# Performance work log

Hardware: AMD Instinct MI355X
Metric: run time of the kernel (lower is better)

## Reference

```python
import jax, jax.numpy as jnp
import numpy as np

N_NODES = 100000
N_EDGES = 3200000
N_FEAT = 128
N_GRAPHS = 1024
N_CLASSES = 10
K = 30  # global_sort_pool k


def setup_inputs() -> dict:
    key = jax.random.key(0)
    ks = jax.random.split(key, 20)
    p = lambda k, shape: jax.random.normal(k, shape, jnp.float32) * 0.1
    return {
        "x": jax.random.normal(ks[0], (N_NODES, N_FEAT), jnp.float32),
        "w1": p(ks[1], (N_FEAT, 32)), "b1": p(ks[2], (32,)),
        "w2": p(ks[3], (32, 32)),     "b2": p(ks[4], (32,)),
        "w3": p(ks[5], (32, 32)),     "b3": p(ks[6], (32,)),
        "w4": p(ks[7], (32, 1)),      "b4": p(ks[8], (1,)),
        "conv5_w": p(ks[9], (16, 1, 97)),  "conv5_b": p(ks[10], (16,)),
        "conv6_w": p(ks[11], (32, 16, 5)), "conv6_b": p(ks[12], (32,)),
        "fc1_w": p(ks[13], (352, 128)),    "fc1_b": p(ks[14], (128,)),
        "fc2_w": p(ks[15], (128, N_CLASSES)), "fc2_b": p(ks[16], (N_CLASSES,)),
        "edge_src": jax.random.randint(ks[17], (N_EDGES,), 0, N_NODES),
        "edge_dst": jax.random.randint(ks[18], (N_EDGES,), 0, N_NODES),
        "batch": jnp.sort(jax.random.randint(ks[19], (N_NODES,), 0, N_GRAPHS)),
        "num_graphs": N_GRAPHS,
    }


def _gcn_forward(x, w1, b1, w2, b2, w3, b3, w4, b4,
                 conv5_w, conv5_b, conv6_w, conv6_b,
                 fc1_w, fc1_b, fc2_w, fc2_b,
                 edge_src, edge_dst, batch, num_graphs):
    n = x.shape[0]
    # remove_self_loops: mask self-loop edges to weight 0 (shapes stay static)
    ew = (edge_src != edge_dst).astype(x.dtype)
    # gcn_norm with added self-loops (weight 1): deg includes self-loop
    deg = jax.ops.segment_sum(ew, edge_dst, num_segments=n) + 1.0
    dis = jax.lax.rsqrt(deg)                       # deg^{-1/2}
    enorm = dis[edge_src] * dis[edge_dst] * ew     # [E]
    snorm = (dis * dis)[:, None]                   # self-loop norm [n,1]

    def gcn_conv(h, W, b):
        h = h @ W                                   # [n, out]
        agg = jax.ops.segment_sum(h[edge_src] * enorm[:, None], edge_dst,
                                  num_segments=n) + h * snorm
        return agg + b

    x1 = jnp.tanh(gcn_conv(x,  w1, b1))   # [n,32]
    x2 = jnp.tanh(gcn_conv(x1, w2, b2))   # [n,32]
    x3 = jnp.tanh(gcn_conv(x2, w3, b3))   # [n,32]
    x4 = jnp.tanh(gcn_conv(x3, w4, b4))   # [n,1]
    xc = jnp.concatenate([x1, x2, x3, x4], axis=-1)  # [n,97]

    # global_sort_pool(k=K): per-graph sort by last channel, descending
    key_last = xc[:, -1]
    order = jnp.lexsort((-key_last, batch))          # primary: batch, secondary: desc key
    bs = batch[order]                                # sorted graph ids
    counts = jax.ops.segment_sum(jnp.ones_like(batch, jnp.int32), batch,
                                 num_segments=num_graphs)
    starts = jnp.cumsum(counts) - counts             # exclusive prefix sum
    rank = jnp.arange(n) - starts[bs]                # rank within own graph
    r = jnp.where(rank < K, rank, K)                 # overflow -> dummy slot K
    pooled = jnp.zeros((num_graphs, K + 1, 97), xc.dtype)
    pooled = pooled.at[bs, r].set(xc[order])
    pooled = pooled[:, :K, :].reshape(num_graphs, 1, K * 97)  # [B,1,2910]

    # Conv1d(1,16,97,97) + relu
    h = jax.lax.conv_general_dilated(pooled, conv5_w, (97,), 'VALID',
                                     dimension_numbers=('NCH', 'OIH', 'NCH'))
    h = jax.nn.relu(h + conv5_b[None, :, None])      # [B,16,30]
    # MaxPool1d(2,2)
    h = jax.lax.reduce_window(h, -jnp.inf, jax.lax.max,
                              (1, 1, 2), (1, 1, 2), 'VALID')  # [B,16,15]
    # Conv1d(16,32,5,1) + relu
    h = jax.lax.conv_general_dilated(h, conv6_w, (1,), 'VALID',
                                     dimension_numbers=('NCH', 'OIH', 'NCH'))
    h = jax.nn.relu(h + conv6_b[None, :, None])      # [B,32,11]
    h = h.reshape(num_graphs, -1)                    # [B,352]

    h = jax.nn.relu(h @ fc1_w + fc1_b)               # [B,128]; dropout = identity (eval)
    return jax.nn.log_softmax(h @ fc2_w + fc2_b, axis=-1)  # [B,num_classes]


def reference(x, w1, b1, w2, b2, w3, b3, w4, b4,
              conv5_w, conv5_b, conv6_w, conv6_b,
              fc1_w, fc1_b, fc2_w, fc2_b,
              edge_src, edge_dst, batch, num_graphs):
    return _gcn_forward(x, w1, b1, w2, b2, w3, b3, w4, b4,
                        conv5_w, conv5_b, conv6_w, conv6_b,
                        fc1_w, fc1_b, fc2_w, fc2_b,
                        edge_src, edge_dst, batch, num_graphs)
```

## Files before the change

### kernel.cpp

```cpp
#include <hip/hip_runtime.h>
#include <hip/hip_bf16.h>

#define N_NODES 100000
#define N_EDGES 3200000
#define NGRAPH 1024
#define KTOP 30
#define PELEM (NGRAPH * KTOP * 97)

#define NBKT 782
#define NTILE 391
#define TILE 8192
#define BKT_CAP 4736

typedef __hip_bfloat16 bf16;
typedef float vfloat4 __attribute__((ext_vector_type(4)));

__device__ __forceinline__ float u2f(unsigned short h) {
    return __uint_as_float(((unsigned int)h) << 16);
}
__device__ __forceinline__ float LD(const void* p, int i, int bf) {
    if (bf) return u2f(((const unsigned short*)p)[i]);
    return ((const float*)p)[i];
}

__global__ void k_detect(const void* w1, int* flag) {
    if (threadIdx.x == 0 && blockIdx.x == 0) {
        const unsigned short* u = (const unsigned short*)w1;
        int plausible = 0;
        for (int i = 0; i < 64; i++) {
            float a = fabsf(u2f(u[2 * i]));
            if (a == 0.f || (a >= 9.765625e-4f && a <= 2.0f)) plausible++;
        }
        *flag = (plausible >= 40) ? 1 : 0;
    }
}

__global__ void k_icur(int* __restrict__ cur) {
    int i = blockIdx.x * 256 + threadIdx.x;
    if (i < NBKT) cur[i] = i * BKT_CAP;
}

__global__ __launch_bounds__(256) void k_scat(const int* __restrict__ src,
                                              const int* __restrict__ dst,
                                              int* __restrict__ cur,
                                              int* __restrict__ ebuf) {
    __shared__ int pk[TILE];
    __shared__ unsigned short bk[TILE];
    __shared__ int h[NBKT];
    __shared__ int base[NBKT];
    int tid = threadIdx.x;
    int ebase = blockIdx.x * TILE;
    for (int i = tid; i < NBKT; i += 256) h[i] = 0;
    __syncthreads();
    for (int i = tid; i < TILE; i += 256) {
        int e = ebase + i;
        int bkt = 0xFFFF;
        if (e < N_EDGES) {
            int s = __builtin_nontemporal_load(src + e);
            int d = __builtin_nontemporal_load(dst + e);
            if (s != d) {
                bkt = d >> 7;
                pk[i] = ((d & 127) << 17) | s;
                atomicAdd(&h[bkt], 1);
            }
        }
        bk[i] = (unsigned short)bkt;
    }
    __syncthreads();
    for (int i = tid; i < NBKT; i += 256) {
        int c = h[i];
        base[i] = c ? atomicAdd(&cur[i], c) : 0;
    }
    __syncthreads();
    for (int i = tid; i < NBKT; i += 256) h[i] = 0;
    __syncthreads();
    for (int i = tid; i < TILE; i += 256) {
        int bkt = bk[i];
        if (bkt != 0xFFFF) {
            int p = base[bkt] + atomicAdd(&h[bkt], 1);
            if (p < (bkt + 1) * BKT_CAP) ebuf[p] = pk[i];
        }
    }
}

__global__ __launch_bounds__(256) void k_bcsr(const int* __restrict__ ebuf,
                                              const int* __restrict__ cur,
                                              int* __restrict__ rs,
                                              int* __restrict__ re,
                                              float* __restrict__ dis,
                                              int* __restrict__ csr) {
    __shared__ int dloc[128];
    __shared__ int sc[128];
    int b = blockIdx.x;
    int node0 = b << 7;
    int nn = N_NODES - node0; if (nn > 128) nn = 128;
    int tid = threadIdx.x;
    if (tid < 128) dloc[tid] = 0;
    __syncthreads();
    int s = b * BKT_CAP;
    int cnt = cur[b] - s; if (cnt > BKT_CAP) cnt = BKT_CAP;
    int e = s + cnt;
    for (int i = s + tid; i < e; i += 256)
        atomicAdd(&dloc[ebuf[i] >> 17], 1);
    __syncthreads();
    if (tid < 128) sc[tid] = dloc[tid];
    __syncthreads();
    for (int off = 1; off < 128; off <<= 1) {
        int t = (tid >= off && tid < 128) ? sc[tid - off] : 0;
        __syncthreads();
        if (tid < 128) sc[tid] += t;
        __syncthreads();
    }
    if (tid < nn) {
        int st = s + sc[tid] - dloc[tid];
        rs[node0 + tid] = st;
        re[node0 + tid] = st + dloc[tid];
        dis[node0 + tid] = rsqrtf((float)dloc[tid] + 1.0f);
    }
    __syncthreads();
    if (tid < 128) dloc[tid] = s + sc[tid] - dloc[tid];
    __syncthreads();
    for (int i = s + tid; i < e; i += 256) {
        int pv = ebuf[i];
        int pos = atomicAdd(&dloc[pv >> 17], 1);
        csr[pos] = pv & 0x1FFFF;
    }
}

__global__ void k_gstart(const int* __restrict__ batch, int* __restrict__ gstart) {
    int g = blockIdx.x * 256 + threadIdx.x;
    if (g > NGRAPH) return;
    int lo = 0, hi = N_NODES;
    while (lo < hi) {
        int mid = (lo + hi) >> 1;
        if (batch[mid] < g) lo = mid + 1; else hi = mid;
    }
    gstart[g] = lo;
}

__global__ __launch_bounds__(256) void k_mm1(const void* __restrict__ x,
                                             const void* __restrict__ w,
                                             const int* __restrict__ flagp,
                                             const float* __restrict__ dis,
                                             float* __restrict__ ts) {
    __shared__ float Wl[128 * 32];
    __shared__ float Xs[32][128];
    int bf = *flagp;
    int tid = threadIdx.x;
    int nbase = blockIdx.x * 32;
    if (bf) {
        const ushort4* wv = (const ushort4*)w;
        for (int idx = tid; idx < 1024; idx += 256) {
            ushort4 h = wv[idx];
            int p = idx * 4;
            Wl[p] = u2f(h.x); Wl[p + 1] = u2f(h.y); Wl[p + 2] = u2f(h.z); Wl[p + 3] = u2f(h.w);
        }
        const ushort4* xv = (const ushort4*)x;
        for (int idx = tid; idx < 1024; idx += 256) {
            int nd = idx >> 5, q = idx & 31;
            ushort4 h = xv[(size_t)(nbase + nd) * 32 + q];
            float* d = &Xs[nd][q * 4];
            d[0] = u2f(h.x); d[1] = u2f(h.y); d[2] = u2f(h.z); d[3] = u2f(h.w);
        }
    } else {
        const float* wf = (const float*)w;
        for (int idx = tid; idx < 4096; idx += 256) Wl[idx] = wf[idx];
        const float* xf = (const float*)x;
        for (int idx = tid; idx < 4096; idx += 256)
            Xs[idx >> 7][idx & 127] = xf[(size_t)nbase * 128 + idx];
    }
    __syncthreads();
    int grp = tid >> 5, col = tid & 31;
    for (int rep = 0; rep < 4; rep++) {
        int sub = grp + 8 * rep;
        int node = nbase + sub;
        float acc = 0.f;
#pragma unroll 8
        for (int k = 0; k < 128; k++) acc += Xs[sub][k] * Wl[k * 32 + col];
        ts[node * 32 + col] = dis[node] * acc;
    }
}

template<int OUTF>
__global__ __launch_bounds__(256) void k_aggf(const float4* __restrict__ ts,
                                              const int* __restrict__ rs,
                                              const int* __restrict__ re,
                                              const int* __restrict__ csr,
                                              const float* __restrict__ dis,
                                              const void* __restrict__ b,
                                              const void* __restrict__ Wn,
                                              const int* __restrict__ flagp,
                                              float4* __restrict__ out,
                                              float* __restrict__ tsn) {
    __shared__ float Wl[OUTF == 1 ? 32 : 1024];
    __shared__ float Xrow[4][32];
    int tid = threadIdx.x;
    int bf = *flagp;
    if (OUTF == 32) {
        if (bf) {
            ushort4 h = ((const ushort4*)Wn)[tid];
            int p = tid * 4;
            Wl[p] = u2f(h.x); Wl[p + 1] = u2f(h.y); Wl[p + 2] = u2f(h.z); Wl[p + 3] = u2f(h.w);
        } else {
            float4 v = ((const float4*)Wn)[tid];
            int p = tid * 4;
            Wl[p] = v.x; Wl[p + 1] = v.y; Wl[p + 2] = v.z; Wl[p + 3] = v.w;
        }
    } else {
        if (tid < 32) Wl[tid] = LD(Wn, tid, bf);
    }

    int wid = tid >> 6;
    int node = blockIdx.x * 4 + wid;
    int lane = tid & 63;
    int q   = lane & 7;
    int grp = lane >> 3;
    int s = rs[node], e = re[node];
    float4 a0 = make_float4(0.f, 0.f, 0.f, 0.f);
    float4 a1 = a0, a2 = a0, a3 = a0;
    int i = s + grp;
    for (; i + 24 < e; i += 32) {
        int v0 = csr[i], v1 = csr[i + 8], v2 = csr[i + 16], v3 = csr[i + 24];
        float4 m0 = ts[v0 * 8 + q];
        float4 m1 = ts[v1 * 8 + q];
        float4 m2 = ts[v2 * 8 + q];
        float4 m3 = ts[v3 * 8 + q];
        a0.x += m0.x; a0.y += m0.y; a0.z += m0.z; a0.w += m0.w;
        a1.x += m1.x; a1.y += m1.y; a1.z += m1.z; a1.w += m1.w;
        a2.x += m2.x; a2.y += m2.y; a2.z += m2.z; a2.w += m2.w;
        a3.x += m3.x; a3.y += m3.y; a3.z += m3.z; a3.w += m3.w;
    }
    for (; i < e; i += 8) {
        float4 m = ts[csr[i] * 8 + q];
        a0.x += m.x; a0.y += m.y; a0.z += m.z; a0.w += m.w;
    }
    float4 acc;
    acc.x = (a0.x + a1.x) + (a2.x + a3.x);
    acc.y = (a0.y + a1.y) + (a2.y + a3.y);
    acc.z = (a0.z + a1.z) + (a2.z + a3.z);
    acc.w = (a0.w + a1.w) + (a2.w + a3.w);
#pragma unroll
    for (int off = 8; off < 64; off <<= 1) {
        acc.x += __shfl_xor(acc.x, off);
        acc.y += __shfl_xor(acc.y, off);
        acc.z += __shfl_xor(acc.z, off);
        acc.w += __shfl_xor(acc.w, off);
    }
    if (grp == 0) {
        float4 self = ts[node * 8 + q];
        float d = dis[node];
        vfloat4 r;
        r.x = tanhf(d * (acc.x + self.x) + LD(b, q * 4 + 0, bf));
        r.y = tanhf(d * (acc.y + self.y) + LD(b, q * 4 + 1, bf));
        r.z = tanhf(d * (acc.z + self.z) + LD(b, q * 4 + 2, bf));
        r.w = tanhf(d * (acc.w + self.w) + LD(b, q * 4 + 3, bf));
        __builtin_nontemporal_store(r, (vfloat4*)&out[node * 8 + q]);
        Xrow[wid][q * 4 + 0] = r.x;
        Xrow[wid][q * 4 + 1] = r.y;
        Xrow[wid][q * 4 + 2] = r.z;
        Xrow[wid][q * 4 + 3] = r.w;
    }
    __syncthreads();
    if (OUTF == 32) {
        int nd = tid >> 6;
        int col = tid & 31;
        int kbase = (tid & 32) >> 1;
        const float* xr = Xrow[nd];
        float a = 0.f;
#pragma unroll
        for (int k2 = 0; k2 < 16; k2++) a += xr[kbase + k2] * Wl[(kbase + k2) * 32 + col];
        a += __shfl_xor(a, 32);
        if (!(tid & 32)) {
            int n2 = blockIdx.x * 4 + nd;
            tsn[n2 * 32 + col] = dis[n2] * a;
        }
    } else {
        int g8 = tid >> 5;
        if (g8 < 4) {
            int n2 = blockIdx.x * 4 + g8;
            int k = tid & 31;
            float a = Xrow[g8][k] * Wl[k];
#pragma unroll
            for (int off = 16; off; off >>= 1) a += __shfl_xor(a, off);
            if (k == 0) tsn[n2] = dis[n2] * a;
        }
    }
}

__global__ __launch_bounds__(256) void k_agg1(const float* __restrict__ ts4,
                                              const int* __restrict__ rs,
                                              const int* __restrict__ re,
                                              const int* __restrict__ csr,
                                              const float* __restrict__ dis,
                                              const void* __restrict__ b4,
                                              const int* __restrict__ flagp,
                                              float* __restrict__ x4) {
    int node = blockIdx.x * 16 + (threadIdx.x >> 4);
    int lane = threadIdx.x & 15;
    int s = rs[node], e = re[node];
    float acc = 0.f;
    for (int i = s + lane; i < e; i += 16) acc += ts4[csr[i]];
#pragma unroll
    for (int off = 1; off < 16; off <<= 1) acc += __shfl_xor(acc, off);
    if (lane == 0) {
        int bf = *flagp;
        x4[node] = tanhf(dis[node] * (acc + ts4[node]) + LD(b4, 0, bf));
    }
}

__global__ __launch_bounds__(256) void k_rank(const int* __restrict__ batch,
                                              const int* __restrict__ gstart,
                                              const float* __restrict__ x4,
                                              int* __restrict__ sel) {
    int i = blockIdx.x * 256 + threadIdx.x;
    if (i >= N_NODES) return;
    int g = batch[i];
    int s = gstart[g], e = gstart[g + 1];
    float ki = x4[i];
    int rank = 0;
    for (int j = s; j < e; j++) {
        float kj = x4[j];
        rank += (kj > ki) || (kj == ki && j < i);
    }
    if (rank < KTOP) sel[g * KTOP + rank] = i;
}

__global__ __launch_bounds__(256) void k_pool(const float* __restrict__ x1,
                                              const float* __restrict__ x2,
                                              const float* __restrict__ x3,
                                              const float* __restrict__ x4,
                                              const int* __restrict__ sel,
                                              float* __restrict__ P) {
    int idx = blockIdx.x * 256 + threadIdx.x;
    if (idx >= PELEM) return;
    int g = idx / (KTOP * 97);
    int r = idx - g * (KTOP * 97);
    int p = r / 97;
    int f = r - p * 97;
    int v = sel[g * KTOP + p];
    float val = 0.f;
    if (v >= 0) {
        if (f < 32)      val = x1[v * 32 + f];
        else if (f < 64) val = x2[v * 32 + f - 32];
        else if (f < 96) val = x3[v * 32 + f - 64];
        else             val = x4[v];
    }
    P[idx] = val;
}

__global__ __launch_bounds__(256) void k_head(
    const float* __restrict__ Pg,
    const void* __restrict__ w5, const void* __restrict__ b5,
    const void* __restrict__ w6, const void* __restrict__ b6,
    const void* __restrict__ f1w, const void* __restrict__ f1b,
    const void* __restrict__ f2w, const void* __restrict__ f2b,
    const int* __restrict__ flagp, void* __restrict__ out) {
    __shared__ float P[KTOP * 97];
    __shared__ float W5[16 * 97];
    __shared__ float W6[32 * 16 * 5];
    __shared__ float H5[16][30];
    __shared__ float M[16][15];
    __shared__ float H6[352];
    __shared__ float Rp[256];
    __shared__ float R1[128];
    __shared__ float L[10];
    __shared__ float mls;
    int g = blockIdx.x;
    int tid = threadIdx.x;
    int bf = *flagp;

    for (int i = tid; i < KTOP * 97; i += 256) P[i] = Pg[g * (KTOP * 97) + i];
    if (bf) {
        const ushort4* w5v = (const ushort4*)w5;
        for (int i = tid; i < 388; i += 256) {
            ushort4 h = w5v[i];
            int p = i * 4;
            W5[p] = u2f(h.x); W5[p + 1] = u2f(h.y); W5[p + 2] = u2f(h.z); W5[p + 3] = u2f(h.w);
        }
        const ushort4* w6v = (const ushort4*)w6;
        for (int i = tid; i < 640; i += 256) {
            ushort4 h = w6v[i];
            int p = i * 4;
            W6[p] = u2f(h.x); W6[p + 1] = u2f(h.y); W6[p + 2] = u2f(h.z); W6[p + 3] = u2f(h.w);
        }
    } else {
        for (int i = tid; i < 16 * 97; i += 256) W5[i] = ((const float*)w5)[i];
        for (int i = tid; i < 2560; i += 256) W6[i] = ((const float*)w6)[i];
    }
    __syncthreads();
    for (int idx = tid; idx < 480; idx += 256) {
        int o = idx / 30, p = idx - o * 30;
        float acc = LD(b5, o, bf);
        const float* pr = &P[p * 97];
        const float* wr = &W5[o * 97];
        for (int f = 0; f < 97; f++) acc += wr[f] * pr[f];
        H5[o][p] = fmaxf(acc, 0.f);
    }
    __syncthreads();
    for (int idx = tid; idx < 240; idx += 256) {
        int o = idx / 15, q = idx - o * 15;
        M[o][q] = fmaxf(H5[o][2 * q], H5[o][2 * q + 1]);
    }
    __syncthreads();
    for (int idx = tid; idx < 352; idx += 256) {
        int oc = idx / 11, tp = idx - oc * 11;
        float acc = LD(b6, oc, bf);
        const float* wr = &W6[oc * 80];
        for (int ic = 0; ic < 16; ic++) {
#pragma unroll
            for (int k = 0; k < 5; k++)
                acc += wr[ic * 5 + k] * M[ic][tp + k];
        }
        H6[idx] = fmaxf(acc, 0.f);
    }
    __syncthreads();
    {
        int half = tid >> 7, col = tid & 127;
        int base = half * 176;
        float a = 0.f;
        for (int i = 0; i < 176; i++) {
            int ii = base + i;
            a += H6[ii] * LD(f1w, ii * 128 + col, bf);
        }
        Rp[tid] = a;
    }
    __syncthreads();
    if (tid < 128) R1[tid] = fmaxf(LD(f1b, tid, bf) + Rp[tid] + Rp[128 + tid], 0.f);
    __syncthreads();
    if (tid < 10) {
        float acc = LD(f2b, tid, bf);
        for (int k = 0; k < 128; k++) acc += R1[k] * LD(f2w, k * 10 + tid, bf);
        L[tid] = acc;
    }
    __syncthreads();
    if (tid == 0) {
        float m = L[0];
        for (int c = 1; c < 10; c++) m = fmaxf(m, L[c]);
        float ssum = 0.f;
        for (int c = 0; c < 10; c++) ssum += expf(L[c] - m);
        mls = m + logf(ssum);
    }
    __syncthreads();
    if (tid < 10) {
        float v = L[tid] - mls;
        if (bf) ((bf16*)out)[g * 10 + tid] = __float2bfloat16(v);
        else    ((float*)out)[g * 10 + tid] = v;
    }
}

extern "C" void kernel_launch(void* const* d_in, const int* in_sizes, int n_in,
                              void* d_out, int out_size, void* d_ws, size_t ws_size,
                              hipStream_t stream) {
    const void* x   = d_in[0];
    const void* w1  = d_in[1];  const void* b1  = d_in[2];
    const void* w2  = d_in[3];  const void* b2  = d_in[4];
    const void* w3  = d_in[5];  const void* b3  = d_in[6];
    const void* w4  = d_in[7];  const void* b4  = d_in[8];
    const void* w5  = d_in[9];  const void* b5  = d_in[10];
    const void* w6  = d_in[11]; const void* b6  = d_in[12];
    const void* f1w = d_in[13]; const void* f1b = d_in[14];
    const void* f2w = d_in[15]; const void* f2b = d_in[16];
    const int* esrc  = (const int*)d_in[17];
    const int* edst  = (const int*)d_in[18];
    const int* batch = (const int*)d_in[19];

    char* w = (char*)d_ws;
    size_t off = 0;
    auto alloc = [&](size_t bytes) {
        void* p = w + off;
        off += (bytes + 255) & ~(size_t)255;
        return p;
    };
    int*   flag   = (int*)  alloc(256);
    int*   rs     = (int*)  alloc((size_t)N_NODES * 4);
    int*   re     = (int*)  alloc((size_t)N_NODES * 4);
    float* dis    = (float*)alloc((size_t)N_NODES * 4);
    int*   csr    = (int*)  alloc((size_t)NBKT * BKT_CAP * 4);
    float* t      = (float*)alloc((size_t)N_NODES * 32 * 4);
    float* t2     = (float*)alloc((size_t)N_NODES * 32 * 4);
    float* x1     = (float*)alloc((size_t)N_NODES * 32 * 4);
    float* x2     = (float*)alloc((size_t)N_NODES * 32 * 4);
    float* x3     = (float*)alloc((size_t)N_NODES * 32 * 4);
    float* x4     = (float*)alloc((size_t)N_NODES * 4);
    int*   gstart = (int*)  alloc((size_t)(NGRAPH + 1) * 4);
    int*   sel    = (int*)  alloc((size_t)NGRAPH * KTOP * 4);
    float* Pg     = (float*)alloc((size_t)PELEM * 4);
    int*   cur    = (int*)  alloc((size_t)NBKT * 4);
    (void)ws_size; (void)n_in; (void)in_sizes; (void)out_size;

    int* ebuf = (int*)t;

    (void)hipMemsetAsync(sel, 0xFF, (size_t)NGRAPH * KTOP * 4, stream);

    int nb   = (N_NODES + 255) / 256;
    int mb32 = N_NODES / 32;
    int ab   = N_NODES / 4;
    int a1b  = N_NODES / 16;
    int pb   = (PELEM + 255) / 256;

    k_detect<<<1, 64, 0, stream>>>(w1, flag);
    k_icur<<<(NBKT + 255) / 256, 256, 0, stream>>>(cur);
    k_scat<<<NTILE, 256, 0, stream>>>(esrc, edst, cur, ebuf);
    k_bcsr<<<NBKT, 256, 0, stream>>>(ebuf, cur, rs, re, dis, csr);
    k_gstart<<<5, 256, 0, stream>>>(batch, gstart);

    k_mm1<<<mb32, 256, 0, stream>>>(x, w1, flag, dis, t);
    k_aggf<32><<<ab, 256, 0, stream>>>((const float4*)t,  rs, re, csr, dis, b1, w2, flag, (float4*)x1, t2);
    k_aggf<32><<<ab, 256, 0, stream>>>((const float4*)t2, rs, re, csr, dis, b2, w3, flag, (float4*)x2, t);
    k_aggf<1><<<ab, 256, 0, stream>>>((const float4*)t,  rs, re, csr, dis, b3, w4, flag, (float4*)x3, t2);
    k_agg1<<<a1b, 256, 0, stream>>>(t2, rs, re, csr, dis, b4, flag, x4);
    k_rank<<<nb, 256, 0, stream>>>(batch, gstart, x4, sel);
    k_pool<<<pb, 256, 0, stream>>>(x1, x2, x3, x4, sel, Pg);
    k_head<<<NGRAPH, 256, 0, stream>>>(Pg, w5, b5, w6, b6,
                                       f1w, f1b, f2w, f2b, flag, (void*)d_out);
}
```

Measured before the change: 587.2 us.

## Aggregate previous layer output directly and apply weights after aggregation

Changes GCN layers 2 and 3 to aggregate the previous activations, scaled per neighbor by dis, and to multiply by W only after aggregation (A·X·W order). This removes the separate pre-transformed t/t2 buffers and the write of those intermediates. In exchange, every edge in the gather loop now does an extra random dis[v] load. The first layer keeps the old order. The layer-4 projection is folded into the layer-3 epilogue, and the nontemporal output store becomes a plain store.

```diff
diff --git a/kernel.cpp b/kernel.cpp
--- a/kernel.cpp
+++ b/kernel.cpp
@@ -13,7 +13,6 @@
 #define BKT_CAP 4736
 
 typedef __hip_bfloat16 bf16;
-typedef float vfloat4 __attribute__((ext_vector_type(4)));
 
 __device__ __forceinline__ float u2f(unsigned short h) {
     return __uint_as_float(((unsigned int)h) << 16);
@@ -181,40 +180,19 @@
     }
 }
 
-template<int OUTF>
-__global__ __launch_bounds__(256) void k_aggf(const float4* __restrict__ ts,
-                                              const int* __restrict__ rs,
-                                              const int* __restrict__ re,
-                                              const int* __restrict__ csr,
-                                              const float* __restrict__ dis,
-                                              const void* __restrict__ b,
-                                              const void* __restrict__ Wn,
-                                              const int* __restrict__ flagp,
-                                              float4* __restrict__ out,
-                                              float* __restrict__ tsn) {
-    __shared__ float Wl[OUTF == 1 ? 32 : 1024];
-    __shared__ float Xrow[4][32];
-    int tid = threadIdx.x;
-    int bf = *flagp;
-    if (OUTF == 32) {
-        if (bf) {
-            ushort4 h = ((const ushort4*)Wn)[tid];
-            int p = tid * 4;
-            Wl[p] = u2f(h.x); Wl[p + 1] = u2f(h.y); Wl[p + 2] = u2f(h.z); Wl[p + 3] = u2f(h.w);
-        } else {
-            float4 v = ((const float4*)Wn)[tid];
-            int p = tid * 4;
-            Wl[p] = v.x; Wl[p + 1] = v.y; Wl[p + 2] = v.z; Wl[p + 3] = v.w;
-        }
-    } else {
-        if (tid < 32) Wl[tid] = LD(Wn, tid, bf);
-    }
-
-    int wid = tid >> 6;
-    int node = blockIdx.x * 4 + wid;
-    int lane = tid & 63;
+__global__ __launch_bounds__(256) void k_agg(const float4* __restrict__ ts,
+                                             const int* __restrict__ rs,
+                                             const int* __restrict__ re,
+                                             const int* __restrict__ csr,
+                                             const float* __restrict__ dis,
+                                             const void* __restrict__ b,
+                                             const int* __restrict__ flagp,
+                                             float4* __restrict__ out) {
+    int node = blockIdx.x * 4 + (threadIdx.x >> 6);
+    int lane = threadIdx.x & 63;
     int q   = lane & 7;
     int grp = lane >> 3;
+    int bf = *flagp;
     int s = rs[node], e = re[node];
     float4 a0 = make_float4(0.f, 0.f, 0.f, 0.f);
     float4 a1 = a0, a2 = a0, a3 = a0;
@@ -249,41 +227,108 @@
     if (grp == 0) {
         float4 self = ts[node * 8 + q];
         float d = dis[node];
-        vfloat4 r;
+        float4 r;
         r.x = tanhf(d * (acc.x + self.x) + LD(b, q * 4 + 0, bf));
         r.y = tanhf(d * (acc.y + self.y) + LD(b, q * 4 + 1, bf));
         r.z = tanhf(d * (acc.z + self.z) + LD(b, q * 4 + 2, bf));
         r.w = tanhf(d * (acc.w + self.w) + LD(b, q * 4 + 3, bf));
-        __builtin_nontemporal_store(r, (vfloat4*)&out[node * 8 + q]);
-        Xrow[wid][q * 4 + 0] = r.x;
-        Xrow[wid][q * 4 + 1] = r.y;
-        Xrow[wid][q * 4 + 2] = r.z;
-        Xrow[wid][q * 4 + 3] = r.w;
-    }
-    __syncthreads();
-    if (OUTF == 32) {
-        int nd = tid >> 6;
-        int col = tid & 31;
-        int kbase = (tid & 32) >> 1;
-        const float* xr = Xrow[nd];
-        float a = 0.f;
+        out[node * 8 + q] = r;
+    }
+}
+
+template<int DO_TS4>
+__global__ __launch_bounds__(256) void k_aggz(const float4* __restrict__ xin,
+                                              const int* __restrict__ rs,
+                                              const int* __restrict__ re,
+                                              const int* __restrict__ csr,
+                                              const float* __restrict__ dis,
+                                              const void* __restrict__ W,
+                                              const void* __restrict__ b,
+                                              const void* __restrict__ w4,
+                                              const int* __restrict__ flagp,
+                                              float* __restrict__ xout,
+                                              float* __restrict__ ts4) {
+    __shared__ float Wl[1024];
+    __shared__ float W4l[32];
+    __shared__ float Z[4][32];
+    int tid = threadIdx.x;
+    int bf = *flagp;
+    if (bf) {
+        ushort4 h = ((const ushort4*)W)[tid];
+        int p = tid * 4;
+        Wl[p] = u2f(h.x); Wl[p + 1] = u2f(h.y); Wl[p + 2] = u2f(h.z); Wl[p + 3] = u2f(h.w);
+    } else {
+        float4 v = ((const float4*)W)[tid];
+        int p = tid * 4;
+        Wl[p] = v.x; Wl[p + 1] = v.y; Wl[p + 2] = v.z; Wl[p + 3] = v.w;
+    }
+    if (DO_TS4 && tid < 32) W4l[tid] = LD(w4, tid, bf);
+
+    int wid = tid >> 6;
+    int node = blockIdx.x * 4 + wid;
+    int lane = tid & 63;
+    int q   = lane & 7;
+    int grp = lane >> 3;
+    int s = rs[node], e = re[node];
+    float4 a0 = make_float4(0.f, 0.f, 0.f, 0.f);
+    float4 a1 = a0, a2 = a0, a3 = a0;
+    int i = s + grp;
+    for (; i + 24 < e; i += 32) {
+        int v0 = csr[i], v1 = csr[i + 8], v2 = csr[i + 16], v3 = csr[i + 24];
+        float d0 = dis[v0], d1 = dis[v1], d2 = dis[v2], d3 = dis[v3];
+        float4 m0 = xin[v0 * 8 + q];
+        float4 m1 = xin[v1 * 8 + q];
+        float4 m2 = xin[v2 * 8 + q];
+        float4 m3 = xin[v3 * 8 + q];
+        a0.x += d0 * m0.x; a0.y += d0 * m0.y; a0.z += d0 * m0.z; a0.w += d0 * m0.w;
+        a1.x += d1 * m1.x; a1.y += d1 * m1.y; a1.z += d1 * m1.z; a1.w += d1 * m1.w;
+        a2.x += d2 * m2.x; a2.y += d2 * m2.y; a2.z += d2 * m2.z; a2.w += d2 * m2.w;
+        a3.x += d3 * m3.x; a3.y += d3 * m3.y; a3.z += d3 * m3.z; a3.w += d3 * m3.w;
+    }
+    for (; i < e; i += 8) {
+        int v = csr[i];
+        float dv = dis[v];
+        float4 m = xin[v * 8 + q];
+        a0.x += dv * m.x; a0.y += dv * m.y; a0.z += dv * m.z; a0.w += dv * m.w;
+    }
+    float4 acc;
+    acc.x = (a0.x + a1.x) + (a2.x + a3.x);
+    acc.y = (a0.y + a1.y) + (a2.y + a3.y);
+    acc.z = (a0.z + a1.z) + (a2.z + a3.z);
+    acc.w = (a0.w + a1.w) + (a2.w + a3.w);
 #pragma unroll
-        for (int k2 = 0; k2 < 16; k2++) a += xr[kbase + k2] * Wl[(kbase + k2) * 32 + col];
-        a += __shfl_xor(a, 32);
-        if (!(tid & 32)) {
-            int n2 = blockIdx.x * 4 + nd;
-            tsn[n2 * 32 + col] = dis[n2] * a;
-        }
-    } else {
-        int g8 = tid >> 5;
-        if (g8 < 4) {
-            int n2 = blockIdx.x * 4 + g8;
-            int k = tid & 31;
-            float a = Xrow[g8][k] * Wl[k];
+    for (int off = 8; off < 64; off <<= 1) {
+        acc.x += __shfl_xor(acc.x, off);
+        acc.y += __shfl_xor(acc.y, off);
+        acc.z += __shfl_xor(acc.z, off);
+        acc.w += __shfl_xor(acc.w, off);
+    }
+    if (grp == 0) {
+        float4 self = xin[node * 8 + q];
+        float di = dis[node];
+        Z[wid][q * 4 + 0] = acc.x + di * self.x;
+        Z[wid][q * 4 + 1] = acc.y + di * self.y;
+        Z[wid][q * 4 + 2] = acc.z + di * self.z;
+        Z[wid][q * 4 + 3] = acc.w + di * self.w;
+    }
+    __syncthreads();
+    int nd = tid >> 6;
+    int col = tid & 31;
+    int kbase = (tid & 32) >> 1;
+    const float* zr = Z[nd];
+    float a = 0.f;
 #pragma unroll
-            for (int off = 16; off; off >>= 1) a += __shfl_xor(a, off);
-            if (k == 0) tsn[n2] = dis[n2] * a;
-        }
+    for (int k2 = 0; k2 < 16; k2++) a += zr[kbase + k2] * Wl[(kbase + k2) * 32 + col];
+    a += __shfl_xor(a, 32);
+    int n2 = blockIdx.x * 4 + nd;
+    float di2 = dis[n2];
+    float xo = tanhf(di2 * a + LD(b, col, bf));
+    if (!(tid & 32)) xout[n2 * 32 + col] = xo;
+    if (DO_TS4) {
+        float t4 = xo * W4l[col];
+#pragma unroll
+        for (int off = 1; off < 32; off <<= 1) t4 += __shfl_xor(t4, off);
+        if ((tid & 63) == 0) ts4[n2] = di2 * t4;
     }
 }
 
@@ -477,11 +522,11 @@
     float* dis    = (float*)alloc((size_t)N_NODES * 4);
     int*   csr    = (int*)  alloc((size_t)NBKT * BKT_CAP * 4);
     float* t      = (float*)alloc((size_t)N_NODES * 32 * 4);
-    float* t2     = (float*)alloc((size_t)N_NODES * 32 * 4);
     float* x1     = (float*)alloc((size_t)N_NODES * 32 * 4);
     float* x2     = (float*)alloc((size_t)N_NODES * 32 * 4);
     float* x3     = (float*)alloc((size_t)N_NODES * 32 * 4);
     float* x4     = (float*)alloc((size_t)N_NODES * 4);
+    float* ts4b   = (float*)alloc((size_t)N_NODES * 4);
     int*   gstart = (int*)  alloc((size_t)(NGRAPH + 1) * 4);
     int*   sel    = (int*)  alloc((size_t)NGRAPH * KTOP * 4);
     float* Pg     = (float*)alloc((size_t)PELEM * 4);
@@ -505,10 +550,10 @@
     k_gstart<<<5, 256, 0, stream>>>(batch, gstart);
 
     k_mm1<<<mb32, 256, 0, stream>>>(x, w1, flag, dis, t);
-    k_aggf<32><<<ab, 256, 0, stream>>>((const float4*)t,  rs, re, csr, dis, b1, w2, flag, (float4*)x1, t2);
-    k_aggf<32><<<ab, 256, 0, stream>>>((const float4*)t2, rs, re, csr, dis, b2, w3, flag, (float4*)x2, t);
-    k_aggf<1><<<ab, 256, 0, stream>>>((const float4*)t,  rs, re, csr, dis, b3, w4, flag, (float4*)x3, t2);
-    k_agg1<<<a1b, 256, 0, stream>>>(t2, rs, re, csr, dis, b4, flag, x4);
+    k_agg<<<ab, 256, 0, stream>>>((const float4*)t, rs, re, csr, dis, b1, flag, (float4*)x1);
+    k_aggz<0><<<ab, 256, 0, stream>>>((const float4*)x1, rs, re, csr, dis, w2, b2, w4, flag, x2, ts4b);
+    k_aggz<1><<<ab, 256, 0, stream>>>((const float4*)x2, rs, re, csr, dis, w3, b3, w4, flag, x3, ts4b);
+    k_agg1<<<a1b, 256, 0, stream>>>(ts4b, rs, re, csr, dis, b4, flag, x4);
     k_rank<<<nb, 256, 0, stream>>>(batch, gstart, x4, sel);
     k_pool<<<pb, 256, 0, stream>>>(x1, x2, x3, x4, sel, Pg);
     k_head<<<NGRAPH, 256, 0, stream>>>(Pg, w5, b5, w6, b6,
```

Result: faster. 561.8 us (-4.3%).
